# Kernel tuning notes

Hardware: AMD Instinct MI355X
Metric: run time of the kernel (lower is better)

Reference implementation:

```python
import jax, jax.numpy as jnp
import numpy as np

B, N_IN, N_OUT = 8192, 2048, 2048


def setup_inputs() -> dict:
    key = jax.random.key(0)
    kx, kw = jax.random.split(key)
    x = jax.random.normal(kx, (B, N_IN), dtype=jnp.float32)
    # torch: uniform_(-0.5, 0.5)
    weight = jax.random.uniform(kw, (N_IN, N_OUT), dtype=jnp.float32, minval=-0.5, maxval=0.5)
    return {"x": x, "weight": weight}


def reference(x, weight):
    # Binarize: W > 0 -> {0, 1}; then dense matmul (batch, n_in) @ (n_in, n_out)
    w_bin = (weight > 0).astype(x.dtype)
    return x @ w_bin
```

## Files before the change

### kernel.cpp

```cpp
#include <hip/hip_runtime.h>


#define MDIM 8192
#define NDIM 2048
#define KDIM 2048
#define NT   (KDIM / 128)

typedef __attribute__((ext_vector_type(8))) short short8;
typedef __attribute__((ext_vector_type(4))) float float4v;
typedef __attribute__((ext_vector_type(4))) float f32x4;
typedef __attribute__((ext_vector_type(4))) int int4v;
typedef __attribute__((ext_vector_type(4))) unsigned short ushort4v;
typedef __attribute__((ext_vector_type(8))) unsigned short ushort8v;

__device__ __forceinline__ unsigned short f2bf(float f) {
    union { float f; unsigned u; } v; v.f = f;
    unsigned r = v.u + 0x7FFFu + ((v.u >> 16) & 1u);
    return (unsigned short)(r >> 16);
}

__device__ __forceinline__ void gload_lds16(void* l, const void* g) {
    __builtin_amdgcn_global_load_lds(
        (const __attribute__((address_space(1))) unsigned int*)g,
        (__attribute__((address_space(3))) unsigned int*)l,
        16, 0, 0);
}

#define FENCE asm volatile("" ::: "memory")
#define BAR do { FENCE; __builtin_amdgcn_s_barrier(); FENCE; } while (0)

__global__ __launch_bounds__(256) void prep(const float* __restrict__ X,
                                            const float* __restrict__ W,
                                            signed char* __restrict__ Xq,
                                            signed char* __restrict__ Wt,
                                            float* __restrict__ Sc) {
    __shared__ __align__(16) signed char T[64][80];
    __shared__ float wm[4];
    const int t = threadIdx.x;
    const int bid = blockIdx.x;

    if (bid < MDIM) {
        const int row = bid;
        const float* xr = X + (size_t)row * KDIM + t * 8;
        float4v a = *reinterpret_cast<const float4v*>(xr);
        float4v b = *reinterpret_cast<const float4v*>(xr + 4);
        float m = fabsf(a[0]);
        m = fmaxf(m, fabsf(a[1])); m = fmaxf(m, fabsf(a[2])); m = fmaxf(m, fabsf(a[3]));
        m = fmaxf(m, fabsf(b[0])); m = fmaxf(m, fabsf(b[1]));
        m = fmaxf(m, fabsf(b[2])); m = fmaxf(m, fabsf(b[3]));
#pragma unroll
        for (int off = 32; off; off >>= 1)
            m = fmaxf(m, __shfl_xor(m, off));
        if ((t & 63) == 0) wm[t >> 6] = m;
        __syncthreads();
        const float s = fmaxf(fmaxf(wm[0], wm[1]), fmaxf(wm[2], wm[3]));
        const float inv = (s > 0.f) ? 127.0f / s : 0.f;

        int q[8];
        q[0] = __float2int_rn(a[0] * inv); q[1] = __float2int_rn(a[1] * inv);
        q[2] = __float2int_rn(a[2] * inv); q[3] = __float2int_rn(a[3] * inv);
        q[4] = __float2int_rn(b[0] * inv); q[5] = __float2int_rn(b[1] * inv);
        q[6] = __float2int_rn(b[2] * inv); q[7] = __float2int_rn(b[3] * inv);
        unsigned lo = (q[0] & 255) | ((q[1] & 255) << 8) | ((q[2] & 255) << 16) | ((unsigned)(q[3] & 255) << 24);
        unsigned hi = (q[4] & 255) | ((q[5] & 255) << 8) | ((q[6] & 255) << 16) | ((unsigned)(q[7] & 255) << 24);
        unsigned* dst = (unsigned*)(Xq + (size_t)row * KDIM + t * 8);
        dst[0] = lo; dst[1] = hi;
        if (t == 0) Sc[row] = s * (1.0f / 127.0f);
    } else {
        const int wb = bid - MDIM;
        const int k0 = (wb >> 5) * 64;
        const int n0 = (wb & 31) * 64;
        const int kr = t >> 4;
        const int nc = (t & 15) * 4;
#pragma unroll
        for (int rr = 0; rr < 4; ++rr) {
            int k = k0 + rr * 16 + kr;
            float4v w4 = *reinterpret_cast<const float4v*>(W + (size_t)k * NDIM + n0 + nc);
#pragma unroll
            for (int c = 0; c < 4; ++c)
                T[nc + c][rr * 16 + kr] = (w4[c] > 0.0f) ? (signed char)1 : (signed char)0;
        }
        __syncthreads();
        const int row = t >> 2, ch = t & 3;
        int4v v = *reinterpret_cast<const int4v*>(&T[row][ch * 16]);
        *reinterpret_cast<int4v*>(Wt + (size_t)(n0 + row) * KDIM + k0 + ch * 16) = v;
    }
}

__global__ __launch_bounds__(256, 2) void gemm128(const signed char* __restrict__ A,
                                                  const signed char* __restrict__ Bt,
                                                  const float* __restrict__ Sc,
                                                  float* __restrict__ O) {
    extern __shared__ char lds[];
    const int tid  = threadIdx.x;
    const int lane = tid & 63;
    const int w    = tid >> 6;
    const int wm_  = w >> 1;
    const int wn_  = w & 1;

    int id  = blockIdx.x;
    int swz = (id & 7) * 128 + (id >> 3);
    const int bm = swz >> 4;
    const int bn = swz & 15;

    const int l3 = lane >> 3, l7 = lane & 7;
    const int srcOff = (w * 8 + l3) * KDIM + ((l7 ^ l3) << 4);
    const char* gA = (const char*)A + (size_t)(bm * 128) * KDIM + srcOff;
    const char* gB = (const char*)Bt + (size_t)(bn * 128) * KDIM + srcOff;

    const int fr = lane & 15, fg = lane >> 4;
    const int se0 = ((fg)     ^ (fr & 7)) << 4;
    const int se1 = ((4 + fg) ^ (fr & 7)) << 4;
    const int aRd = (wm_ * 64 + fr) * 128;
    const int bRd = 16384 + (wn_ * 64 + fr) * 128;

    int4v acc[4][4];
#pragma unroll
    for (int i = 0; i < 4; ++i)
#pragma unroll
        for (int j = 0; j < 4; ++j) {
            acc[i][j][0] = 0; acc[i][j][1] = 0; acc[i][j][2] = 0; acc[i][j][3] = 0;
        }

#pragma unroll
    for (int i = 0; i < 4; ++i)
        gload_lds16(lds + i * 4096 + w * 1024, gA + (size_t)i * 32 * KDIM);
#pragma unroll
    for (int i = 0; i < 4; ++i)
        gload_lds16(lds + 16384 + i * 4096 + w * 1024, gB + (size_t)i * 32 * KDIM);

    for (int t = 0; t < NT; ++t) {
        const int cur = (t & 1) << 15;
        const int nxt = ((t + 1) & 1) << 15;
        const bool more = (t + 1 < NT);
        const char* gAs = gA + (size_t)(t + 1) * 128;
        const char* gBs = gB + (size_t)(t + 1) * 128;

        asm volatile("s_waitcnt vmcnt(0)" ::: "memory");
        BAR;

        if (more) {
#pragma unroll
            for (int i = 0; i < 4; ++i)
                gload_lds16(lds + nxt + i * 4096 + w * 1024, gAs + (size_t)i * 32 * KDIM);
#pragma unroll
            for (int i = 0; i < 4; ++i)
                gload_lds16(lds + nxt + 16384 + i * 4096 + w * 1024, gBs + (size_t)i * 32 * KDIM);
        }

        int4v bfr[4][2], af[4][2];
#pragma unroll
        for (int n = 0; n < 4; ++n) {
            bfr[n][0] = *reinterpret_cast<const int4v*>(lds + cur + bRd + n * 2048 + se0);
            bfr[n][1] = *reinterpret_cast<const int4v*>(lds + cur + bRd + n * 2048 + se1);
        }
#pragma unroll
        for (int m = 0; m < 4; ++m) {
            af[m][0] = *reinterpret_cast<const int4v*>(lds + cur + aRd + m * 2048 + se0);
            af[m][1] = *reinterpret_cast<const int4v*>(lds + cur + aRd + m * 2048 + se1);
        }
        __builtin_amdgcn_s_setprio(1);
#pragma unroll
        for (int m = 0; m < 4; ++m)
#pragma unroll
            for (int n = 0; n < 4; ++n) {
                acc[m][n] = __builtin_amdgcn_mfma_i32_16x16x64_i8(af[m][0], bfr[n][0], acc[m][n], 0, 0, 0);
                acc[m][n] = __builtin_amdgcn_mfma_i32_16x16x64_i8(af[m][1], bfr[n][1], acc[m][n], 0, 0, 0);
            }
        __builtin_amdgcn_s_setprio(0);
    }

    const int orow0 = bm * 128 + wm_ * 64 + fg * 4;
    const int ocol0 = bn * 128 + wn_ * 64 + fr;
#pragma unroll
    for (int mi = 0; mi < 4; ++mi)
#pragma unroll
        for (int r = 0; r < 4; ++r) {
            const int row = orow0 + mi * 16 + r;
            const float s = Sc[row];
            float* op = O + (size_t)row * NDIM + ocol0;
#pragma unroll
            for (int ni = 0; ni < 4; ++ni)
                op[ni * 16] = s * (float)acc[mi][ni][r];
        }
}

__global__ __launch_bounds__(256, 2) void binlin_fused(
        const float* __restrict__ X, const float* __restrict__ W,
        float* __restrict__ O) {
    const int tid = threadIdx.x;
    const int lane = tid & 63;
    const int wave = tid >> 6;
    const int wr = wave >> 1, wc = wave & 1;
    const int NWG = (MDIM / 128) * (NDIM / 128);
    int id = blockIdx.x;
    int swz = (id & 7) * (NWG >> 3) + (id >> 3);
    const int bm = swz >> 4, bn = swz & 15;

    __shared__ __align__(16) unsigned short As[128][40];
    __shared__ __align__(16) unsigned short Bs[128][40];

    const int rA = tid >> 3, kA = (tid & 7) * 4;
    const float* aPtr = X + (size_t)(bm * 128 + rA) * KDIM + kA;
    const int nB = (tid & 31) * 4, kB = (tid >> 5) * 4;
    const float* bPtr = W + (size_t)kB * NDIM + (size_t)bn * 128 + nB;

    float4v aReg[4], bReg[4];
#pragma unroll
    for (int p = 0; p < 4; ++p)
        aReg[p] = *reinterpret_cast<const float4v*>(aPtr + (size_t)(32 * p) * KDIM);
#pragma unroll
    for (int dk = 0; dk < 4; ++dk)
        bReg[dk] = *reinterpret_cast<const float4v*>(bPtr + (size_t)dk * NDIM);

    f32x4 acc[4][4];
#pragma unroll
    for (int i = 0; i < 4; ++i)
#pragma unroll
        for (int j = 0; j < 4; ++j) {
            acc[i][j][0] = 0.f; acc[i][j][1] = 0.f; acc[i][j][2] = 0.f; acc[i][j][3] = 0.f;
        }

    const int r16 = lane & 15, g8 = (lane >> 4) * 8;
    for (int kt = 0; kt < KDIM; kt += 32) {
#pragma unroll
        for (int p = 0; p < 4; ++p) {
            ushort4v v;
            v[0] = f2bf(aReg[p][0]); v[1] = f2bf(aReg[p][1]);
            v[2] = f2bf(aReg[p][2]); v[3] = f2bf(aReg[p][3]);
            *reinterpret_cast<ushort4v*>(&As[rA + 32 * p][kA]) = v;
        }
        unsigned short bb[4][4];
#pragma unroll
        for (int dk = 0; dk < 4; ++dk)
#pragma unroll
            for (int dn = 0; dn < 4; ++dn)
                bb[dn][dk] = (bReg[dk][dn] > 0.0f) ? (unsigned short)0x3F80u
                                                   : (unsigned short)0u;
#pragma unroll
        for (int dn = 0; dn < 4; ++dn) {
            ushort4v v;
            v[0] = bb[dn][0]; v[1] = bb[dn][1]; v[2] = bb[dn][2]; v[3] = bb[dn][3];
            *reinterpret_cast<ushort4v*>(&Bs[nB + dn][kB]) = v;
        }
        __syncthreads();
        if (kt + 32 < KDIM) {
#pragma unroll
            for (int p = 0; p < 4; ++p)
                aReg[p] = *reinterpret_cast<const float4v*>(
                    aPtr + (size_t)(32 * p) * KDIM + (kt + 32));
#pragma unroll
            for (int dk = 0; dk < 4; ++dk)
                bReg[dk] = *reinterpret_cast<const float4v*>(
                    bPtr + (size_t)(kt + 32 + dk) * NDIM);
        }
        short8 af[4], bf[4];
#pragma unroll
        for (int mi = 0; mi < 4; ++mi)
            af[mi] = *reinterpret_cast<const short8*>(&As[wr * 64 + mi * 16 + r16][g8]);
#pragma unroll
        for (int ni = 0; ni < 4; ++ni)
            bf[ni] = *reinterpret_cast<const short8*>(&Bs[wc * 64 + ni * 16 + r16][g8]);
#pragma unroll
        for (int mi = 0; mi < 4; ++mi)
#pragma unroll
            for (int ni = 0; ni < 4; ++ni)
                acc[mi][ni] = __builtin_amdgcn_mfma_f32_16x16x32_bf16(
                    af[mi], bf[ni], acc[mi][ni], 0, 0, 0);
        __syncthreads();
    }

    const int orow0 = bm * 128 + wr * 64 + (lane >> 4) * 4;
    const int ocol0 = bn * 128 + wc * 64 + r16;
#pragma unroll
    for (int mi = 0; mi < 4; ++mi)
#pragma unroll
        for (int ni = 0; ni < 4; ++ni)
#pragma unroll
            for (int r = 0; r < 4; ++r)
                O[(size_t)(orow0 + mi * 16 + r) * NDIM + ocol0 + ni * 16] =
                    acc[mi][ni][r];
}

extern "C" void kernel_launch(void* const* d_in, const int* in_sizes, int n_in,
                              void* d_out, int out_size, void* d_ws, size_t ws_size,
                              hipStream_t stream) {
    const float* X = (const float*)d_in[0];
    const float* W = (const float*)d_in[1];
    float* O = (float*)d_out;
    (void)in_sizes; (void)n_in; (void)out_size;

    const size_t xq_bytes = (size_t)MDIM * KDIM;
    const size_t wt_bytes = (size_t)NDIM * KDIM;
    const size_t sc_bytes = (size_t)MDIM * sizeof(float);
    const size_t need = xq_bytes + wt_bytes + sc_bytes;

    if (ws_size >= need) {
        signed char* Xq = (signed char*)d_ws;
        signed char* Wt = Xq + xq_bytes;
        float* Sc = (float*)(Wt + wt_bytes);
        hipFuncSetAttribute((const void*)gemm128,
                            hipFuncAttributeMaxDynamicSharedMemorySize, 65536);
        prep<<<dim3(MDIM + (KDIM / 64) * (NDIM / 64)), dim3(256), 0, stream>>>(X, W, Xq, Wt, Sc);
        gemm128<<<dim3((MDIM / 128) * (NDIM / 128)), dim3(256), 65536, stream>>>(Xq, Wt, Sc, O);
    } else {
        binlin_fused<<<dim3((MDIM / 128) * (NDIM / 128)), dim3(256), 0, stream>>>(X, W, O);
    }
}
```

Before: 58.38 us.

## Replace LDS-staged int8 GEMM with register-direct global loads on 256x256 tiles

Rewrites the int8 GEMM to drop LDS staging entirely: each wave loads its MFMA operand fragments straight from global memory into registers. Loads for the next K step are interleaved between two halves of the MFMA work as a register double buffer. The block tile grows to 256x256 with 512 threads and 8x4 accumulators per wave. This removes LDS traffic and barriers, but global loads with a 2 KB row stride are poorly coalesced, fragments are re-read across waves through cache instead of shared memory, and register pressure rises.

```diff
diff --git a/kernel.cpp b/kernel.cpp
--- a/kernel.cpp
+++ b/kernel.cpp
@@ -19,15 +19,7 @@
     return (unsigned short)(r >> 16);
 }
 
-__device__ __forceinline__ void gload_lds16(void* l, const void* g) {
-    __builtin_amdgcn_global_load_lds(
-        (const __attribute__((address_space(1))) unsigned int*)g,
-        (__attribute__((address_space(3))) unsigned int*)l,
-        16, 0, 0);
-}
-
 #define FENCE asm volatile("" ::: "memory")
-#define BAR do { FENCE; __builtin_amdgcn_s_barrier(); FENCE; } while (0)
 
 __global__ __launch_bounds__(256) void prep(const float* __restrict__ X,
                                             const float* __restrict__ W,
@@ -87,93 +79,110 @@
     }
 }
 
-__global__ __launch_bounds__(256, 2) void gemm128(const signed char* __restrict__ A,
-                                                  const signed char* __restrict__ Bt,
-                                                  const float* __restrict__ Sc,
-                                                  float* __restrict__ O) {
-    extern __shared__ char lds[];
+__global__ __launch_bounds__(512, 2) void gemm_tex(const signed char* __restrict__ A,
+                                                   const signed char* __restrict__ Bt,
+                                                   const float* __restrict__ Sc,
+                                                   float* __restrict__ O) {
     const int tid  = threadIdx.x;
     const int lane = tid & 63;
     const int w    = tid >> 6;
-    const int wm_  = w >> 1;
-    const int wn_  = w & 1;
+    const int wr   = w >> 2;
+    const int wc   = w & 3;
 
     int id  = blockIdx.x;
-    int swz = (id & 7) * 128 + (id >> 3);
-    const int bm = swz >> 4;
-    const int bn = swz & 15;
-
-    const int l3 = lane >> 3, l7 = lane & 7;
-    const int srcOff = (w * 8 + l3) * KDIM + ((l7 ^ l3) << 4);
-    const char* gA = (const char*)A + (size_t)(bm * 128) * KDIM + srcOff;
-    const char* gB = (const char*)Bt + (size_t)(bn * 128) * KDIM + srcOff;
+    int swz = (id & 7) * 32 + (id >> 3);
+    const int bm = swz >> 3;
+    const int bn = swz & 7;
 
     const int fr = lane & 15, fg = lane >> 4;
-    const int se0 = ((fg)     ^ (fr & 7)) << 4;
-    const int se1 = ((4 + fg) ^ (fr & 7)) << 4;
-    const int aRd = (wm_ * 64 + fr) * 128;
-    const int bRd = 16384 + (wn_ * 64 + fr) * 128;
-
-    int4v acc[4][4];
-#pragma unroll
-    for (int i = 0; i < 4; ++i)
+    const char* aB = (const char*)A + (size_t)(bm * 256 + wr * 128 + fr) * KDIM + fg * 16;
+    const char* bB = (const char*)Bt + (size_t)(bn * 256 + wc * 64 + fr) * KDIM + fg * 16;
+
+    int4v acc[8][4];
+#pragma unroll
+    for (int i = 0; i < 8; ++i)
 #pragma unroll
         for (int j = 0; j < 4; ++j) {
             acc[i][j][0] = 0; acc[i][j][1] = 0; acc[i][j][2] = 0; acc[i][j][3] = 0;
         }
 
-#pragma unroll
-    for (int i = 0; i < 4; ++i)
-        gload_lds16(lds + i * 4096 + w * 1024, gA + (size_t)i * 32 * KDIM);
-#pragma unroll
-    for (int i = 0; i < 4; ++i)
-        gload_lds16(lds + 16384 + i * 4096 + w * 1024, gB + (size_t)i * 32 * KDIM);
+    int4v a1[4][2], a2[4][2], bf[4][2];
+
+#pragma unroll
+    for (int mi = 0; mi < 4; ++mi)
+#pragma unroll
+        for (int ks = 0; ks < 2; ++ks)
+            a1[mi][ks] = *reinterpret_cast<const int4v*>(aB + (size_t)mi * 16 * KDIM + ks * 64);
+    FENCE;
+#pragma unroll
+    for (int ni = 0; ni < 4; ++ni)
+#pragma unroll
+        for (int ks = 0; ks < 2; ++ks)
+            bf[ni][ks] = *reinterpret_cast<const int4v*>(bB + (size_t)ni * 16 * KDIM + ks * 64);
+    FENCE;
+#pragma unroll
+    for (int mi = 0; mi < 4; ++mi)
+#pragma unroll
+        for (int ks = 0; ks < 2; ++ks)
+            a2[mi][ks] = *reinterpret_cast<const int4v*>(aB + (size_t)(4 + mi) * 16 * KDIM + ks * 64);
+    FENCE;
 
     for (int t = 0; t < NT; ++t) {
-        const int cur = (t & 1) << 15;
-        const int nxt = ((t + 1) & 1) << 15;
         const bool more = (t + 1 < NT);
-        const char* gAs = gA + (size_t)(t + 1) * 128;
-        const char* gBs = gB + (size_t)(t + 1) * 128;
-
-        asm volatile("s_waitcnt vmcnt(0)" ::: "memory");
-        BAR;
-
-        if (more) {
-#pragma unroll
-            for (int i = 0; i < 4; ++i)
-                gload_lds16(lds + nxt + i * 4096 + w * 1024, gAs + (size_t)i * 32 * KDIM);
-#pragma unroll
-            for (int i = 0; i < 4; ++i)
-                gload_lds16(lds + nxt + 16384 + i * 4096 + w * 1024, gBs + (size_t)i * 32 * KDIM);
-        }
-
-        int4v bfr[4][2], af[4][2];
-#pragma unroll
-        for (int n = 0; n < 4; ++n) {
-            bfr[n][0] = *reinterpret_cast<const int4v*>(lds + cur + bRd + n * 2048 + se0);
-            bfr[n][1] = *reinterpret_cast<const int4v*>(lds + cur + bRd + n * 2048 + se1);
-        }
-#pragma unroll
-        for (int m = 0; m < 4; ++m) {
-            af[m][0] = *reinterpret_cast<const int4v*>(lds + cur + aRd + m * 2048 + se0);
-            af[m][1] = *reinterpret_cast<const int4v*>(lds + cur + aRd + m * 2048 + se1);
-        }
+        const char* aN = aB + (size_t)(t + 1) * 128;
+        const char* bN = bB + (size_t)(t + 1) * 128;
+
         __builtin_amdgcn_s_setprio(1);
 #pragma unroll
-        for (int m = 0; m < 4; ++m)
-#pragma unroll
-            for (int n = 0; n < 4; ++n) {
-                acc[m][n] = __builtin_amdgcn_mfma_i32_16x16x64_i8(af[m][0], bfr[n][0], acc[m][n], 0, 0, 0);
-                acc[m][n] = __builtin_amdgcn_mfma_i32_16x16x64_i8(af[m][1], bfr[n][1], acc[m][n], 0, 0, 0);
+        for (int mi = 0; mi < 4; ++mi)
+#pragma unroll
+            for (int ni = 0; ni < 4; ++ni) {
+                acc[mi][ni] = __builtin_amdgcn_mfma_i32_16x16x64_i8(a1[mi][0], bf[ni][0], acc[mi][ni], 0, 0, 0);
+                acc[mi][ni] = __builtin_amdgcn_mfma_i32_16x16x64_i8(a1[mi][1], bf[ni][1], acc[mi][ni], 0, 0, 0);
             }
         __builtin_amdgcn_s_setprio(0);
+        FENCE;
+
+        if (more) {
+#pragma unroll
+            for (int mi = 0; mi < 4; ++mi)
+#pragma unroll
+                for (int ks = 0; ks < 2; ++ks)
+                    a1[mi][ks] = *reinterpret_cast<const int4v*>(aN + (size_t)mi * 16 * KDIM + ks * 64);
+        }
+        FENCE;
+
+        __builtin_amdgcn_s_setprio(1);
+#pragma unroll
+        for (int mi = 0; mi < 4; ++mi)
+#pragma unroll
+            for (int ni = 0; ni < 4; ++ni) {
+                acc[4 + mi][ni] = __builtin_amdgcn_mfma_i32_16x16x64_i8(a2[mi][0], bf[ni][0], acc[4 + mi][ni], 0, 0, 0);
+                acc[4 + mi][ni] = __builtin_amdgcn_mfma_i32_16x16x64_i8(a2[mi][1], bf[ni][1], acc[4 + mi][ni], 0, 0, 0);
+            }
+        __builtin_amdgcn_s_setprio(0);
+        FENCE;
+
+        if (more) {
+#pragma unroll
+            for (int ni = 0; ni < 4; ++ni)
+#pragma unroll
+                for (int ks = 0; ks < 2; ++ks)
+                    bf[ni][ks] = *reinterpret_cast<const int4v*>(bN + (size_t)ni * 16 * KDIM + ks * 64);
+            FENCE;
+#pragma unroll
+            for (int mi = 0; mi < 4; ++mi)
+#pragma unroll
+                for (int ks = 0; ks < 2; ++ks)
+                    a2[mi][ks] = *reinterpret_cast<const int4v*>(aN + (size_t)(4 + mi) * 16 * KDIM + ks * 64);
+        }
+        FENCE;
     }
 
-    const int orow0 = bm * 128 + wm_ * 64 + fg * 4;
-    const int ocol0 = bn * 128 + wn_ * 64 + fr;
-#pragma unroll
-    for (int mi = 0; mi < 4; ++mi)
+    const int orow0 = bm * 256 + wr * 128 + fg * 4;
+    const int ocol0 = bn * 256 + wc * 64 + fr;
+#pragma unroll
+    for (int mi = 0; mi < 8; ++mi)
 #pragma unroll
         for (int r = 0; r < 4; ++r) {
             const int row = orow0 + mi * 16 + r;
@@ -254,19 +263,19 @@
                 bReg[dk] = *reinterpret_cast<const float4v*>(
                     bPtr + (size_t)(kt + 32 + dk) * NDIM);
         }
-        short8 af[4], bf[4];
+        short8 af[4], bfv[4];
 #pragma unroll
         for (int mi = 0; mi < 4; ++mi)
             af[mi] = *reinterpret_cast<const short8*>(&As[wr * 64 + mi * 16 + r16][g8]);
 #pragma unroll
         for (int ni = 0; ni < 4; ++ni)
-            bf[ni] = *reinterpret_cast<const short8*>(&Bs[wc * 64 + ni * 16 + r16][g8]);
+            bfv[ni] = *reinterpret_cast<const short8*>(&Bs[wc * 64 + ni * 16 + r16][g8]);
 #pragma unroll
         for (int mi = 0; mi < 4; ++mi)
 #pragma unroll
             for (int ni = 0; ni < 4; ++ni)
                 acc[mi][ni] = __builtin_amdgcn_mfma_f32_16x16x32_bf16(
-                    af[mi], bf[ni], acc[mi][ni], 0, 0, 0);
+                    af[mi], bfv[ni], acc[mi][ni], 0, 0, 0);
         __syncthreads();
     }
 
@@ -299,10 +308,8 @@
         signed char* Xq = (signed char*)d_ws;
         signed char* Wt = Xq + xq_bytes;
         float* Sc = (float*)(Wt + wt_bytes);
-        hipFuncSetAttribute((const void*)gemm128,
-                            hipFuncAttributeMaxDynamicSharedMemorySize, 65536);
         prep<<<dim3(MDIM + (KDIM / 64) * (NDIM / 64)), dim3(256), 0, stream>>>(X, W, Xq, Wt, Sc);
-        gemm128<<<dim3((MDIM / 128) * (NDIM / 128)), dim3(256), 65536, stream>>>(Xq, Wt, Sc, O);
+        gemm_tex<<<dim3((MDIM / 256) * (NDIM / 256)), dim3(512), 0, stream>>>(Xq, Wt, Sc, O);
     } else {
         binlin_fused<<<dim3((MDIM / 128) * (NDIM / 128)), dim3(256), 0, stream>>>(X, W, O);
     }
```

Result: slower. 112.3 us (+92.4%).
